# Performance work log

Hardware: AMD Instinct MI355X
Metric: run time of the kernel (lower is better)

Reference implementation:

```python
import jax, jax.numpy as jnp
import numpy as np

PARENTS = np.array([-1, 0, 1, 1, 1])
NECK_CHAIN = np.array([1, 0])  # neck joint (1) up to root (0)
B, V, F, J, S, E = 512, 5023, 9976, 5, 100, 50
L_STAT, L_DYN, L_FULL, N_BUCKET = 51, 17, 68, 79


def rodrigues(rvec):
    """Axis-angle [N,3] -> rotation matrices [N,3,3]."""
    angle = jnp.linalg.norm(rvec + 1e-8, axis=-1, keepdims=True)  # [N,1]
    axis = rvec / angle
    s = jnp.sin(angle)[..., None]
    c = jnp.cos(angle)[..., None]
    rx, ry, rz = axis[:, 0], axis[:, 1], axis[:, 2]
    z = jnp.zeros_like(rx)
    K = jnp.stack([z, -rz, ry, rz, z, -rx, -ry, rx, z], axis=-1).reshape(-1, 3, 3)
    I = jnp.eye(3, dtype=rvec.dtype)
    return I + s * K + (1.0 - c) * (K @ K)


def verts2lmk(vertices, faces, lmk_faces_idx, lmk_bary):
    lmk_faces = faces[lmk_faces_idx]                               # [B,L,3]
    lmk_verts = jax.vmap(lambda v, f: v[f])(vertices, lmk_faces)   # [B,L,3verts,3xyz]
    return jnp.einsum('blfc,blf->blc', lmk_verts, lmk_bary)


def setup_inputs() -> dict:
    key = jax.random.key(0)
    ks = jax.random.split(key, 16)
    shape_params = jax.random.normal(ks[0], (B, S), jnp.float32)
    expression_params = jax.random.normal(ks[1], (B, E), jnp.float32)
    pose_params = 0.2 * jax.random.normal(ks[2], (B, 6), jnp.float32)
    eye_pose_params = 0.1 * jax.random.normal(ks[3], (B, 6), jnp.float32)
    v_template = jax.random.normal(ks[4], (V, 3), jnp.float32) * 0.1
    shapedirs = jax.random.normal(ks[5], (V, 3, S + E), jnp.float32) * 0.01
    posedirs = jax.random.normal(ks[6], ((J - 1) * 9, V * 3), jnp.float32) * 0.01
    jr = jax.random.uniform(ks[7], (J, V), jnp.float32)
    J_regressor = jr / jnp.sum(jr, axis=1, keepdims=True)
    lbs_weights = jax.nn.softmax(jax.random.normal(ks[8], (V, J), jnp.float32), axis=-1)
    faces = jax.random.randint(ks[9], (F, 3), 0, V)
    lmk_faces_idx = jax.random.randint(ks[10], (L_STAT,), 0, F)
    lb = jax.random.uniform(ks[11], (L_STAT, 3), jnp.float32) + 1e-3
    lmk_bary_coords = lb / jnp.sum(lb, axis=-1, keepdims=True)
    dynamic_lmk_faces_idx = jax.random.randint(ks[12], (N_BUCKET, L_DYN), 0, F)
    db = jax.random.uniform(ks[13], (N_BUCKET, L_DYN, 3), jnp.float32) + 1e-3
    dynamic_lmk_bary_coords = db / jnp.sum(db, axis=-1, keepdims=True)
    full_lmk_faces_idx = jax.random.randint(ks[14], (L_FULL,), 0, F)
    fb = jax.random.uniform(ks[15], (L_FULL, 3), jnp.float32) + 1e-3
    full_lmk_bary_coords = fb / jnp.sum(fb, axis=-1, keepdims=True)
    return {
        'shape_params': shape_params, 'expression_params': expression_params,
        'pose_params': pose_params, 'eye_pose_params': eye_pose_params,
        'v_template': v_template, 'shapedirs': shapedirs, 'posedirs': posedirs,
        'J_regressor': J_regressor, 'lbs_weights': lbs_weights, 'faces': faces,
        'lmk_faces_idx': lmk_faces_idx, 'lmk_bary_coords': lmk_bary_coords,
        'dynamic_lmk_faces_idx': dynamic_lmk_faces_idx,
        'dynamic_lmk_bary_coords': dynamic_lmk_bary_coords,
        'full_lmk_faces_idx': full_lmk_faces_idx,
        'full_lmk_bary_coords': full_lmk_bary_coords,
    }


def reference(shape_params, expression_params, pose_params, eye_pose_params,
              v_template, shapedirs, posedirs, J_regressor, lbs_weights, faces,
              lmk_faces_idx, lmk_bary_coords, dynamic_lmk_faces_idx,
              dynamic_lmk_bary_coords, full_lmk_faces_idx, full_lmk_bary_coords):
    b = shape_params.shape[0]
    nv = v_template.shape[0]
    dt = shape_params.dtype
    betas = jnp.concatenate([shape_params, expression_params], axis=1)          # [B,150]
    neck = jnp.zeros((b, 3), dtype=dt)
    full_pose = jnp.concatenate(
        [pose_params[:, :3], neck, pose_params[:, 3:], eye_pose_params], axis=1)  # [B,15]
    # shape + expression blendshapes
    v_shaped = v_template[None] + jnp.einsum('bl,vcl->bvc', betas, shapedirs)   # [B,V,3]
    joints = jnp.einsum('jv,bvc->bjc', J_regressor, v_shaped)                   # [B,5,3]
    rot_mats = rodrigues(full_pose.reshape(-1, 3)).reshape(b, J, 3, 3)          # [B,5,3,3]
    I3 = jnp.eye(3, dtype=dt)
    pose_feature = (rot_mats[:, 1:] - I3).reshape(b, -1)                        # [B,36]
    v_posed = v_shaped + (pose_feature @ posedirs).reshape(b, nv, 3)
    # kinematic chain -> global joint transforms
    rel_J = joints.at[:, 1:].add(-joints[:, PARENTS[1:]])
    tm = jnp.zeros((b, J, 4, 4), dtype=dt)
    tm = tm.at[:, :, :3, :3].set(rot_mats).at[:, :, :3, 3].set(rel_J).at[:, :, 3, 3].set(1.0)
    chain = [tm[:, 0]]
    for i in range(1, J):
        chain.append(chain[PARENTS[i]] @ tm[:, i])
    A = jnp.stack(chain, axis=1)                                                # [B,5,4,4]
    Rj = jnp.einsum('bjmn,bjn->bjm', A[:, :, :3, :3], joints)
    A_rel = A.at[:, :, :3, 3].add(-Rj)
    # per-vertex skinning
    T = jnp.einsum('vj,bjmn->bvmn', lbs_weights, A_rel)                         # [B,V,4,4]
    vertices = jnp.einsum('bvmn,bvn->bvm', T[:, :, :3, :3], v_posed) + T[:, :, :3, 3]
    # dynamic contour landmark selection from neck kin-chain relative rotation
    aa = full_pose.reshape(b, J, 3)[:, NECK_CHAIN]                              # [B,2,3]
    rc = rodrigues(aa.reshape(-1, 3)).reshape(b, len(NECK_CHAIN), 3, 3)
    rel_rot = jnp.broadcast_to(I3, (b, 3, 3))
    for idx in range(len(NECK_CHAIN)):
        rel_rot = rc[:, idx] @ rel_rot
    sy = jnp.sqrt(rel_rot[:, 0, 0] ** 2 + rel_rot[:, 1, 0] ** 2)
    y_deg = jnp.arctan2(-rel_rot[:, 2, 0], sy) * (180.0 / np.pi)
    y_rot = jnp.round(jnp.minimum(y_deg, 39.0)).astype(jnp.int32)
    neg_mask = y_rot < 0
    big_neg = y_rot < -39
    neg_vals = jnp.where(big_neg, 78, 39 - y_rot)
    y_rot = jnp.where(neg_mask, neg_vals, y_rot)                                # [B] in [0,79)
    dyn_faces = dynamic_lmk_faces_idx[y_rot]                                    # [B,17]
    dyn_bary = dynamic_lmk_bary_coords[y_rot]                                   # [B,17,3]
    lf = jnp.concatenate([dyn_faces, jnp.broadcast_to(lmk_faces_idx[None], (b, lmk_faces_idx.shape[0]))], axis=1)
    lb = jnp.concatenate([dyn_bary, jnp.broadcast_to(lmk_bary_coords[None], (b,) + lmk_bary_coords.shape)], axis=1)
    landmarks2d = verts2lmk(vertices, faces, lf, lb)
    ff = jnp.broadcast_to(full_lmk_faces_idx[None], (b, full_lmk_faces_idx.shape[0]))
    fb = jnp.broadcast_to(full_lmk_bary_coords[None], (b,) + full_lmk_bary_coords.shape)
    landmarks3d = verts2lmk(vertices, faces, ff, fb)
    return (vertices, landmarks2d, landmarks3d)
```

## Files before the change

### kernel.cpp

```cpp
#include <hip/hip_runtime.h>
#include <cstddef>
#include <cstdint>

#define cB   512
#define cV   5023
#define cS   100
#define cE   50
#define cJ   5
#define cLD  17
#define cLF  68

#define cV3    15069
#define cNPAD  15072

#define OUT_V  ((size_t)cB * cV * 3)
#define OUT_L  ((size_t)cB * cLF * 3)

#define WS_BTN    ((size_t)0)
#define WS_ATM    (WS_BTN + (size_t)cNPAD * 96)
#define WS_JS2    (WS_ATM + 49152)
#define WS_AREL   (WS_JS2 + 2432)
#define WS_YROT   (WS_AREL + 30720)
#define WS_JSPART (WS_YROT + 512)

typedef __attribute__((ext_vector_type(8))) short short8;
typedef __attribute__((ext_vector_type(4))) float f32x4;

__device__ __forceinline__ unsigned short f2bf(float x) {
  unsigned int u = __float_as_uint(x);
  u = (u + 0x7fffu + ((u >> 16) & 1u)) >> 16;
  return (unsigned short)u;
}

__device__ __forceinline__ void rodrigues9(float rx, float ry, float rz, float* R) {
  float a0 = rx + 1e-8f, a1 = ry + 1e-8f, a2 = rz + 1e-8f;
  float angle = sqrtf(a0 * a0 + a1 * a1 + a2 * a2);
  float inv = 1.0f / angle;
  float x = rx * inv, y = ry * inv, z = rz * inv;
  float s = sinf(angle), c = cosf(angle);
  float t = 1.0f - c;
  float xy = x * y, xz = x * z, yz = y * z;
  R[0] = 1.0f - t * (y * y + z * z);
  R[1] = -s * z + t * xy;
  R[2] =  s * y + t * xz;
  R[3] =  s * z + t * xy;
  R[4] = 1.0f - t * (x * x + z * z);
  R[5] = -s * x + t * yz;
  R[6] = -s * y + t * xz;
  R[7] =  s * x + t * yz;
  R[8] = 1.0f - t * (x * x + y * y);
}

__global__ __launch_bounds__(512) void k_aux(
    const float* __restrict__ sd, const float* __restrict__ pd,
    const float* __restrict__ jreg, const float* __restrict__ vt,
    unsigned int* __restrict__ btn_u, float* __restrict__ JSpart) {
  __shared__ __align__(16) unsigned char sm[44032];
  float* sdt = (float*)sm;
  unsigned short* pdt = (unsigned short*)(sm + 38912);
  const int t = threadIdx.x;
  const int bid = blockIdx.x;
  if (bid < 314) {
    if (t >= 453) return;
    int c = t / 151, l = t - c * 151;
    int v0 = bid * 16;
    float acc[5] = {0.f, 0.f, 0.f, 0.f, 0.f};
#pragma unroll 8
    for (int vi = 0; vi < 16; ++vi) {
      int v = v0 + vi;
      bool ok = (v < cV);
      int vc = ok ? v : 0;
      float x;
      if (l < 150) x = ok ? sd[(size_t)(v * 3 + c) * 150 + l] : 0.f;
      else         x = ok ? vt[v * 3 + c] : 0.f;
#pragma unroll
      for (int j = 0; j < 5; ++j)
        acc[j] = fmaf(jreg[j * cV + vc], x, acc[j]);
    }
#pragma unroll
    for (int j = 0; j < 5; ++j)
      JSpart[(size_t)bid * 2272 + (j * 3 + c) * 151 + l] = acc[j];
  } else {
    const int n0 = (bid - 314) * 64;
    for (int idx = t; idx < 9600; idx += 512) {
      size_t g = (size_t)n0 * 150 + idx;
      float v = (g < (size_t)cV3 * 150) ? sd[g] : 0.f;
      int row = idx / 150, col = idx - row * 150;
      sdt[row * 152 + col] = v;
    }
    for (int e = t; e < 2304; e += 512) {
      int kk = e >> 6, ln = e & 63;
      int n = n0 + ln;
      pdt[ln * 38 + kk] = f2bf((n < cV3) ? pd[(size_t)kk * cV3 + n] : 0.f);
    }
    __syncthreads();
    for (int e = t; e < 6144; e += 512) {
      int row = e / 96, d = e - row * 96;
      int n = n0 + row;
      if (n < cNPAD) {
        unsigned int wv;
        if (d < 75) {
          wv = (unsigned int)f2bf(sdt[row * 152 + 2 * d]) |
               ((unsigned int)f2bf(sdt[row * 152 + 2 * d + 1]) << 16);
        } else if (d < 93) {
          int p = (d - 75) * 2;
          wv = (unsigned int)pdt[row * 38 + p] |
               ((unsigned int)pdt[row * 38 + p + 1] << 16);
        } else {
          wv = 0u;
        }
        btn_u[(size_t)n * 96 + d] = wv;
      }
    }
  }
}

__global__ __launch_bounds__(256) void k_jsred(const float* __restrict__ JSpart,
                                               float* __restrict__ JS2) {
  __shared__ float red[256];
  const int t = threadIdx.x;
  const int e = blockIdx.x * 32 + (t & 31);
  const int pg = t >> 5;
  float s = 0.f;
  if (e < 2265) {
#pragma unroll 8
    for (int p = pg; p < 314; p += 8)
      s += JSpart[(size_t)p * 2272 + e];
  }
  red[t] = s;
  __syncthreads();
  if (t < 128) red[t] += red[t + 128];
  __syncthreads();
  if (t < 64) red[t] += red[t + 64];
  __syncthreads();
  if (t < 32) {
    float v = red[t] + red[t + 32];
    if (e < 2265) {
      int jc = e / 151, l = e - jc * 151;
      JS2[l * 16 + jc] = v;
    }
  }
}

__global__ __launch_bounds__(256) void k_batch(
    const float* __restrict__ shp, const float* __restrict__ expr,
    const float* __restrict__ pose, const float* __restrict__ eyep,
    const float* __restrict__ JS2g, float* __restrict__ Arel,
    int* __restrict__ yrot, unsigned int* __restrict__ atm_u) {
  __shared__ float js2[151 * 16];
  __shared__ float sb[32 * 153];
  __shared__ float pfs[32 * 36];
  const int t = threadIdx.x;
  const int b0 = blockIdx.x * 32;
  for (int i = t; i < 151 * 16; i += 256) js2[i] = JS2g[i];
  for (int e = t; e < 3200; e += 256) {
    int bl = e / 100, l = e - bl * 100;
    sb[bl * 153 + l] = shp[(size_t)(b0 + bl) * 100 + l];
  }
  for (int e = t; e < 1600; e += 256) {
    int bl = e / 50, l = e - bl * 50;
    sb[bl * 153 + 100 + l] = expr[(size_t)(b0 + bl) * 50 + l];
  }
  __syncthreads();

  if (t < 32) {
    int b = b0 + t;
    float jnt[5][3];
    {
      const f32x4* J4 = (const f32x4*)(js2 + 150 * 16);
      f32x4 A = J4[0], Bq = J4[1], Cq = J4[2], Dq = J4[3];
      jnt[0][0] = A.x;  jnt[0][1] = A.y;  jnt[0][2] = A.z;
      jnt[1][0] = A.w;  jnt[1][1] = Bq.x; jnt[1][2] = Bq.y;
      jnt[2][0] = Bq.z; jnt[2][1] = Bq.w; jnt[2][2] = Cq.x;
      jnt[3][0] = Cq.y; jnt[3][1] = Cq.z; jnt[3][2] = Cq.w;
      jnt[4][0] = Dq.x; jnt[4][1] = Dq.y; jnt[4][2] = Dq.z;
    }
    for (int l = 0; l < 150; ++l) {
      const f32x4* J4 = (const f32x4*)(js2 + l * 16);
      f32x4 A = J4[0], Bq = J4[1], Cq = J4[2], Dq = J4[3];
      float beta = sb[t * 153 + l];
      jnt[0][0] = fmaf(beta, A.x,  jnt[0][0]);
      jnt[0][1] = fmaf(beta, A.y,  jnt[0][1]);
      jnt[0][2] = fmaf(beta, A.z,  jnt[0][2]);
      jnt[1][0] = fmaf(beta, A.w,  jnt[1][0]);
      jnt[1][1] = fmaf(beta, Bq.x, jnt[1][1]);
      jnt[1][2] = fmaf(beta, Bq.y, jnt[1][2]);
      jnt[2][0] = fmaf(beta, Bq.z, jnt[2][0]);
      jnt[2][1] = fmaf(beta, Bq.w, jnt[2][1]);
      jnt[2][2] = fmaf(beta, Cq.x, jnt[2][2]);
      jnt[3][0] = fmaf(beta, Cq.y, jnt[3][0]);
      jnt[3][1] = fmaf(beta, Cq.z, jnt[3][1]);
      jnt[3][2] = fmaf(beta, Cq.w, jnt[3][2]);
      jnt[4][0] = fmaf(beta, Dq.x, jnt[4][0]);
      jnt[4][1] = fmaf(beta, Dq.y, jnt[4][1]);
      jnt[4][2] = fmaf(beta, Dq.z, jnt[4][2]);
    }
    float fp[5][3];
    fp[0][0] = pose[b * 6 + 0]; fp[0][1] = pose[b * 6 + 1]; fp[0][2] = pose[b * 6 + 2];
    fp[1][0] = 0.f; fp[1][1] = 0.f; fp[1][2] = 0.f;
    fp[2][0] = pose[b * 6 + 3]; fp[2][1] = pose[b * 6 + 4]; fp[2][2] = pose[b * 6 + 5];
    fp[3][0] = eyep[b * 6 + 0]; fp[3][1] = eyep[b * 6 + 1]; fp[3][2] = eyep[b * 6 + 2];
    fp[4][0] = eyep[b * 6 + 3]; fp[4][1] = eyep[b * 6 + 4]; fp[4][2] = eyep[b * 6 + 5];
    float R[5][9];
#pragma unroll
    for (int j = 0; j < 5; ++j) rodrigues9(fp[j][0], fp[j][1], fp[j][2], R[j]);
#pragma unroll
    for (int j = 1; j < 5; ++j)
#pragma unroll
      for (int r = 0; r < 9; ++r) {
        float id = (r == 0 || r == 4 || r == 8) ? 1.f : 0.f;
        pfs[t * 36 + (j - 1) * 9 + r] = R[j][r] - id;
      }
    float rel[5][3];
#pragma unroll
    for (int c = 0; c < 3; ++c) {
      rel[0][c] = jnt[0][c];
      rel[1][c] = jnt[1][c] - jnt[0][c];
      rel[2][c] = jnt[2][c] - jnt[1][c];
      rel[3][c] = jnt[3][c] - jnt[1][c];
      rel[4][c] = jnt[4][c] - jnt[1][c];
    }
    float GR[5][9], Gt[5][3];
#pragma unroll
    for (int r = 0; r < 9; ++r) GR[0][r] = R[0][r];
#pragma unroll
    for (int c = 0; c < 3; ++c) Gt[0][c] = rel[0][c];
    const int par[5] = {0, 0, 1, 1, 1};
#pragma unroll
    for (int j = 1; j < 5; ++j) {
      int p = par[j];
#pragma unroll
      for (int r = 0; r < 3; ++r) {
#pragma unroll
        for (int cc = 0; cc < 3; ++cc)
          GR[j][r * 3 + cc] = GR[p][r * 3 + 0] * R[j][0 + cc] +
                              GR[p][r * 3 + 1] * R[j][3 + cc] +
                              GR[p][r * 3 + 2] * R[j][6 + cc];
        Gt[j][r] = Gt[p][r] + GR[p][r * 3 + 0] * rel[j][0] +
                              GR[p][r * 3 + 1] * rel[j][1] +
                              GR[p][r * 3 + 2] * rel[j][2];
      }
    }
#pragma unroll
    for (int j = 0; j < 5; ++j)
#pragma unroll
      for (int r = 0; r < 3; ++r) {
        float tj = Gt[j][r] - (GR[j][r * 3 + 0] * jnt[j][0] +
                               GR[j][r * 3 + 1] * jnt[j][1] +
                               GR[j][r * 3 + 2] * jnt[j][2]);
        Arel[b * 60 + j * 12 + r * 4 + 0] = GR[j][r * 3 + 0];
        Arel[b * 60 + j * 12 + r * 4 + 1] = GR[j][r * 3 + 1];
        Arel[b * 60 + j * 12 + r * 4 + 2] = GR[j][r * 3 + 2];
        Arel[b * 60 + j * 12 + r * 4 + 3] = tj;
      }
    float Ra[9], Rb[9];
    rodrigues9(fp[1][0], fp[1][1], fp[1][2], Ra);
    rodrigues9(fp[0][0], fp[0][1], fp[0][2], Rb);
    float r00 = Rb[0] * Ra[0] + Rb[1] * Ra[3] + Rb[2] * Ra[6];
    float r10 = Rb[3] * Ra[0] + Rb[4] * Ra[3] + Rb[5] * Ra[6];
    float r20 = Rb[6] * Ra[0] + Rb[7] * Ra[3] + Rb[8] * Ra[6];
    float sy = sqrtf(r00 * r00 + r10 * r10);
    float ydeg = atan2f(-r20, sy) * 57.29577951308232f;
    int y = (int)rintf(fminf(ydeg, 39.0f));
    if (y < 0) y = (y < -39) ? 78 : (39 - y);
    yrot[b] = y;
  }
  __syncthreads();

#pragma unroll
  for (int it = 0; it < 12; ++it) {
    int e = t + it * 256;
    int bl = e / 96, d = e - bl * 96;
    unsigned int wv;
    if (d < 75) {
      wv = (unsigned int)f2bf(sb[bl * 153 + 2 * d]) |
           ((unsigned int)f2bf(sb[bl * 153 + 2 * d + 1]) << 16);
    } else if (d < 93) {
      wv = (unsigned int)f2bf(pfs[bl * 36 + (d - 75) * 2]) |
           ((unsigned int)f2bf(pfs[bl * 36 + (d - 75) * 2 + 1]) << 16);
    } else {
      wv = 0u;
    }
    atm_u[(size_t)(b0 + bl) * 96 + d] = wv;
  }
}

__global__ __launch_bounds__(256) void k_main(
    const unsigned short* __restrict__ BTn, const unsigned short* __restrict__ ATm,
    const float* __restrict__ Arel, const float* __restrict__ vtempl,
    const float* __restrict__ lbw, float* __restrict__ out) {
  __shared__ float Pf[96 * 66];
  __shared__ float Os[64 * 97];
  __shared__ float lbwT[160];
  __shared__ float vtT[96];

  const int bid = blockIdx.x;
  const int nb = bid >> 3, mb = bid & 7;

  const int t = threadIdx.x;
  const int w = t >> 6, L = t & 63;
  const int wm = w >> 1, wn = w & 1;
  const int lr = L & 15, lq = L >> 4;

  if (t < 160) {
    int vl = t / 5, j = t - vl * 5;
    int v = nb * 32 + vl;
    lbwT[t] = (v < cV) ? lbw[v * 5 + j] : 0.f;
  }
  if (t >= 160 && t < 256) {
    int e = t - 160;
    int vl = e / 3, c = e - vl * 3;
    int v = nb * 32 + vl;
    vtT[e] = (v < cV) ? vtempl[v * 3 + c] : 0.f;
  }

  const unsigned short* abase = ATm + ((size_t)mb * 64 + wm * 32 + lr) * 192 + lq * 8;
  const unsigned short* bbase = BTn + ((size_t)nb * 96 + wn * 48 + lr) * 192 + lq * 8;

  f32x4 acc[2][3];
#pragma unroll
  for (int mt = 0; mt < 2; ++mt)
#pragma unroll
    for (int nt = 0; nt < 3; ++nt) acc[mt][nt] = (f32x4){0.f, 0.f, 0.f, 0.f};

  short8 A0[3], A1[3], B0[3], B1[3], B2[3];
#pragma unroll
  for (int d = 0; d < 3; ++d) {
    const int ko = d * 32;
    A0[d] = *(const short8*)(abase + ko);
    A1[d] = *(const short8*)(abase + 16 * 192 + ko);
    B0[d] = *(const short8*)(bbase + ko);
    B1[d] = *(const short8*)(bbase + 16 * 192 + ko);
    B2[d] = *(const short8*)(bbase + 32 * 192 + ko);
  }
#pragma unroll
  for (int ks = 0; ks < 6; ++ks) {
    const int d = ks % 3;
    short8 a0 = A0[d], a1 = A1[d], b0 = B0[d], b1 = B1[d], b2 = B2[d];
    if (ks < 3) {
      const int ko = (ks + 3) * 32;
      A0[d] = *(const short8*)(abase + ko);
      A1[d] = *(const short8*)(abase + 16 * 192 + ko);
      B0[d] = *(const short8*)(bbase + ko);
      B1[d] = *(const short8*)(bbase + 16 * 192 + ko);
      B2[d] = *(const short8*)(bbase + 32 * 192 + ko);
    }
    acc[0][0] = __builtin_amdgcn_mfma_f32_16x16x32_bf16(a0, b0, acc[0][0], 0, 0, 0);
    acc[1][0] = __builtin_amdgcn_mfma_f32_16x16x32_bf16(a1, b0, acc[1][0], 0, 0, 0);
    acc[0][1] = __builtin_amdgcn_mfma_f32_16x16x32_bf16(a0, b1, acc[0][1], 0, 0, 0);
    acc[1][1] = __builtin_amdgcn_mfma_f32_16x16x32_bf16(a1, b1, acc[1][1], 0, 0, 0);
    acc[0][2] = __builtin_amdgcn_mfma_f32_16x16x32_bf16(a0, b2, acc[0][2], 0, 0, 0);
    acc[1][2] = __builtin_amdgcn_mfma_f32_16x16x32_bf16(a1, b2, acc[1][2], 0, 0, 0);
  }

#pragma unroll
  for (int mt = 0; mt < 2; ++mt)
#pragma unroll
    for (int nt = 0; nt < 3; ++nt) {
      int n_loc = wn * 48 + nt * 16 + lr;
      int m = wm * 32 + mt * 16 + lq * 4;
      *(f32x4*)(Pf + n_loc * 66 + m) = acc[mt][nt];
    }

  const int b_loc = t >> 2, part = t & 3;
  const float* qb = Arel + ((size_t)mb * 64 + b_loc) * 60;
  f32x4 ar[15];
#pragma unroll
  for (int r = 0; r < 15; ++r) ar[r] = *(const f32x4*)(qb + 4 * r);

  __syncthreads();

#pragma unroll
  for (int ii = 0; ii < 8; ++ii) {
    const int vl = part * 8 + ii;
    float px = Pf[(vl * 3 + 0) * 66 + b_loc] + vtT[vl * 3 + 0];
    float py = Pf[(vl * 3 + 1) * 66 + b_loc] + vtT[vl * 3 + 1];
    float pz = Pf[(vl * 3 + 2) * 66 + b_loc] + vtT[vl * 3 + 2];
    float o0 = 0.f, o1 = 0.f, o2 = 0.f;
#pragma unroll
    for (int j = 0; j < 5; ++j) {
      f32x4 q0 = ar[3 * j + 0], q1 = ar[3 * j + 1], q2 = ar[3 * j + 2];
      float s0 = q0.x * px + q0.y * py + q0.z * pz + q0.w;
      float s1 = q1.x * px + q1.y * py + q1.z * pz + q1.w;
      float s2 = q2.x * px + q2.y * py + q2.z * pz + q2.w;
      float wj = lbwT[vl * 5 + j];
      o0 = fmaf(wj, s0, o0);
      o1 = fmaf(wj, s1, o1);
      o2 = fmaf(wj, s2, o2);
    }
    Os[b_loc * 97 + vl * 3 + 0] = o0;
    Os[b_loc * 97 + vl * 3 + 1] = o1;
    Os[b_loc * 97 + vl * 3 + 2] = o2;
  }
  __syncthreads();

  const size_t cv3 = (size_t)cV * 3;
  const size_t ob = ((size_t)(mb * 64) * cV + (size_t)nb * 32) * 3;
#pragma unroll
  for (int s = 0; s < 24; ++s) {
    int idx = s * 256 + t;
    int bb = idx / 96, f = idx - bb * 96;
    if (nb < 156 || f < 93)
      out[ob + (size_t)bb * cv3 + f] = Os[bb * 97 + f];
  }
}

__global__ __launch_bounds__(512) void k_lmk(
    const float* __restrict__ verts, const int* __restrict__ faces,
    const int* __restrict__ lmkf, const float* __restrict__ lmkb,
    const int* __restrict__ dynf, const float* __restrict__ dynb,
    const int* __restrict__ fullf, const float* __restrict__ fullb,
    const int* __restrict__ yrot, float* __restrict__ out) {
  int id = blockIdx.x * 512 + threadIdx.x;
  if (id >= cB * cLF * 6) return;
  int c = id % 3;
  int q = id / 3;
  int sel = q & 1;
  int r = q >> 1;
  int b = r / cLF, l = r - b * cLF;
  const float* vb = verts + (size_t)b * cV * 3;
  int f; float w0, w1, w2; size_t o;
  if (sel == 0) {
    if (l < cLD) {
      int yb = yrot[b];
      f = dynf[yb * cLD + l];
      const float* bp = dynb + ((size_t)yb * cLD + l) * 3;
      w0 = bp[0]; w1 = bp[1]; w2 = bp[2];
    } else {
      f = lmkf[l - cLD];
      const float* bp = lmkb + (size_t)(l - cLD) * 3;
      w0 = bp[0]; w1 = bp[1]; w2 = bp[2];
    }
    o = OUT_V + ((size_t)b * cLF + l) * 3;
  } else {
    f = fullf[l];
    const float* bp = fullb + (size_t)l * 3;
    w0 = bp[0]; w1 = bp[1]; w2 = bp[2];
    o = OUT_V + OUT_L + ((size_t)b * cLF + l) * 3;
  }
  int i0 = faces[f * 3 + 0] * 3, i1 = faces[f * 3 + 1] * 3, i2 = faces[f * 3 + 2] * 3;
  out[o + c] = w0 * vb[i0 + c] + w1 * vb[i1 + c] + w2 * vb[i2 + c];
}

extern "C" void kernel_launch(void* const* d_in, const int* in_sizes, int n_in,
                              void* d_out, int out_size, void* d_ws, size_t ws_size,
                              hipStream_t stream) {
  (void)in_sizes; (void)n_in; (void)out_size; (void)ws_size;
  const float* shp  = (const float*)d_in[0];
  const float* expr = (const float*)d_in[1];
  const float* pose = (const float*)d_in[2];
  const float* eyep = (const float*)d_in[3];
  const float* vt   = (const float*)d_in[4];
  const float* sd   = (const float*)d_in[5];
  const float* pd   = (const float*)d_in[6];
  const float* jreg = (const float*)d_in[7];
  const float* lbw  = (const float*)d_in[8];
  const int*   fcs  = (const int*)d_in[9];
  const int*   lmkf = (const int*)d_in[10];
  const float* lmkb = (const float*)d_in[11];
  const int*   dynf = (const int*)d_in[12];
  const float* dynb = (const float*)d_in[13];
  const int*   fullf= (const int*)d_in[14];
  const float* fullb= (const float*)d_in[15];
  float* out = (float*)d_out;
  float* ws  = (float*)d_ws;

  unsigned int*   btn  = (unsigned int*)(ws + WS_BTN);
  unsigned short* ATm  = (unsigned short*)(ws + WS_ATM);
  float* JS2    = ws + WS_JS2;
  float* Arel   = ws + WS_AREL;
  int*   yrot   = (int*)(ws + WS_YROT);
  float* JSpart = ws + WS_JSPART;

  k_aux<<<550, 512, 0, stream>>>(sd, pd, jreg, vt, btn, JSpart);
  k_jsred<<<71, 256, 0, stream>>>(JSpart, JS2);
  k_batch<<<16, 256, 0, stream>>>(shp, expr, pose, eyep, JS2, Arel, yrot,
                                  (unsigned int*)ATm);
  k_main<<<1256, 256, 0, stream>>>((unsigned short*)btn, ATm, Arel, vt, lbw, out);
  k_lmk<<<408, 512, 0, stream>>>(out, fcs, lmkf, lmkb, dynf, dynb, fullf, fullb, yrot, out);
}
```

Measured before the change: 174.6 us.

## Fuse five kernels into one persistent cooperative kernel with grid syncs

```diff
diff --git a/kernel.cpp b/kernel.cpp
--- a/kernel.cpp
+++ b/kernel.cpp
@@ -1,6 +1,9 @@
 #include <hip/hip_runtime.h>
+#include <hip/hip_cooperative_groups.h>
 #include <cstddef>
 #include <cstdint>
+
+namespace cg = cooperative_groups;
 
 #define cB   512
 #define cV   5023
@@ -51,53 +54,46 @@
   R[8] = 1.0f - t * (x * x + y * y);
 }
 
-__global__ __launch_bounds__(512) void k_aux(
-    const float* __restrict__ sd, const float* __restrict__ pd,
+__global__ __launch_bounds__(256, 2) void k_fused(
+    const float* __restrict__ sd,   const float* __restrict__ pd,
     const float* __restrict__ jreg, const float* __restrict__ vt,
-    unsigned int* __restrict__ btn_u, float* __restrict__ JSpart) {
-  __shared__ __align__(16) unsigned char sm[44032];
-  float* sdt = (float*)sm;
-  unsigned short* pdt = (unsigned short*)(sm + 38912);
+    const float* __restrict__ shp,  const float* __restrict__ expr,
+    const float* __restrict__ pose, const float* __restrict__ eyep,
+    const float* __restrict__ lbw,  const int* __restrict__ fcs,
+    const int* __restrict__ lmkf,   const float* __restrict__ lmkb,
+    const int* __restrict__ dynf,   const float* __restrict__ dynb,
+    const int* __restrict__ fullf,  const float* __restrict__ fullb,
+    float* __restrict__ out,        unsigned int* __restrict__ btn_u,
+    unsigned short* __restrict__ ATm, float* __restrict__ JS2,
+    float* __restrict__ Arel,       int* __restrict__ yrot,
+    float* __restrict__ JSpart) {
+  cg::grid_group grid = cg::this_grid();
+  __shared__ __align__(16) unsigned char smem[38912];
+
   const int t = threadIdx.x;
-  const int bid = blockIdx.x;
-  if (bid < 314) {
-    if (t >= 453) return;
-    int c = t / 151, l = t - c * 151;
-    int v0 = bid * 16;
-    float acc[5] = {0.f, 0.f, 0.f, 0.f, 0.f};
-#pragma unroll 8
-    for (int vi = 0; vi < 16; ++vi) {
-      int v = v0 + vi;
-      bool ok = (v < cV);
-      int vc = ok ? v : 0;
-      float x;
-      if (l < 150) x = ok ? sd[(size_t)(v * 3 + c) * 150 + l] : 0.f;
-      else         x = ok ? vt[v * 3 + c] : 0.f;
-#pragma unroll
-      for (int j = 0; j < 5; ++j)
-        acc[j] = fmaf(jreg[j * cV + vc], x, acc[j]);
-    }
-#pragma unroll
-    for (int j = 0; j < 5; ++j)
-      JSpart[(size_t)bid * 2272 + (j * 3 + c) * 151 + l] = acc[j];
-  } else {
-    const int n0 = (bid - 314) * 64;
-    for (int idx = t; idx < 9600; idx += 512) {
-      size_t g = (size_t)n0 * 150 + idx;
-      float v = (g < (size_t)cV3 * 150) ? sd[g] : 0.f;
-      int row = idx / 150, col = idx - row * 150;
-      sdt[row * 152 + col] = v;
-    }
-    for (int e = t; e < 2304; e += 512) {
-      int kk = e >> 6, ln = e & 63;
-      int n = n0 + ln;
-      pdt[ln * 38 + kk] = f2bf((n < cV3) ? pd[(size_t)kk * cV3 + n] : 0.f);
-    }
-    __syncthreads();
-    for (int e = t; e < 6144; e += 512) {
-      int row = e / 96, d = e - row * 96;
-      int n = n0 + row;
-      if (n < cNPAD) {
+  const int gtid = blockIdx.x * 256 + t;
+  const int gstride = gridDim.x * 256;
+
+  {
+    float* sdt = (float*)smem;
+    unsigned short* pdt = (unsigned short*)(smem + 19456);
+    for (int vb = blockIdx.x; vb < 471; vb += gridDim.x) {
+      const int n0 = vb * 32;
+      for (int idx = t; idx < 4800; idx += 256) {
+        size_t g = (size_t)n0 * 150 + idx;
+        float v = (g < (size_t)cV3 * 150) ? sd[g] : 0.f;
+        int row = idx / 150, col = idx - row * 150;
+        sdt[row * 152 + col] = v;
+      }
+      for (int e = t; e < 1152; e += 256) {
+        int kk = e >> 5, ln = e & 31;
+        int n = n0 + ln;
+        pdt[ln * 38 + kk] = f2bf((n < cV3) ? pd[(size_t)kk * cV3 + n] : 0.f);
+      }
+      __syncthreads();
+      for (int e = t; e < 3072; e += 256) {
+        int row = e / 96, d = e - row * 96;
+        int n = n0 + row;
         unsigned int wv;
         if (d < 75) {
           wv = (unsigned int)f2bf(sdt[row * 152 + 2 * d]) |
@@ -111,349 +107,385 @@
         }
         btn_u[(size_t)n * 96 + d] = wv;
       }
+      __syncthreads();
     }
   }
-}
-
-__global__ __launch_bounds__(256) void k_jsred(const float* __restrict__ JSpart,
-                                               float* __restrict__ JS2) {
-  __shared__ float red[256];
-  const int t = threadIdx.x;
-  const int e = blockIdx.x * 32 + (t & 31);
-  const int pg = t >> 5;
-  float s = 0.f;
-  if (e < 2265) {
+
+  for (int i = gtid; i < 314 * 453; i += gstride) {
+    int p = i / 453, e = i - p * 453;
+    int c = e / 151, l = e - c * 151;
+    int v0 = p * 16;
+    float acc[5] = {0.f, 0.f, 0.f, 0.f, 0.f};
 #pragma unroll 8
-    for (int p = pg; p < 314; p += 8)
-      s += JSpart[(size_t)p * 2272 + e];
-  }
-  red[t] = s;
-  __syncthreads();
-  if (t < 128) red[t] += red[t + 128];
-  __syncthreads();
-  if (t < 64) red[t] += red[t + 64];
-  __syncthreads();
-  if (t < 32) {
-    float v = red[t] + red[t + 32];
-    if (e < 2265) {
-      int jc = e / 151, l = e - jc * 151;
-      JS2[l * 16 + jc] = v;
+    for (int vi = 0; vi < 16; ++vi) {
+      int v = v0 + vi;
+      bool ok = (v < cV);
+      int vc = ok ? v : 0;
+      float x;
+      if (l < 150) x = ok ? sd[(size_t)(v * 3 + c) * 150 + l] : 0.f;
+      else         x = ok ? vt[v * 3 + c] : 0.f;
+#pragma unroll
+      for (int j = 0; j < 5; ++j)
+        acc[j] = fmaf(jreg[j * cV + vc], x, acc[j]);
     }
-  }
-}
-
-__global__ __launch_bounds__(256) void k_batch(
-    const float* __restrict__ shp, const float* __restrict__ expr,
-    const float* __restrict__ pose, const float* __restrict__ eyep,
-    const float* __restrict__ JS2g, float* __restrict__ Arel,
-    int* __restrict__ yrot, unsigned int* __restrict__ atm_u) {
-  __shared__ float js2[151 * 16];
-  __shared__ float sb[32 * 153];
-  __shared__ float pfs[32 * 36];
-  const int t = threadIdx.x;
-  const int b0 = blockIdx.x * 32;
-  for (int i = t; i < 151 * 16; i += 256) js2[i] = JS2g[i];
-  for (int e = t; e < 3200; e += 256) {
-    int bl = e / 100, l = e - bl * 100;
-    sb[bl * 153 + l] = shp[(size_t)(b0 + bl) * 100 + l];
-  }
-  for (int e = t; e < 1600; e += 256) {
-    int bl = e / 50, l = e - bl * 50;
-    sb[bl * 153 + 100 + l] = expr[(size_t)(b0 + bl) * 50 + l];
-  }
-  __syncthreads();
-
-  if (t < 32) {
-    int b = b0 + t;
-    float jnt[5][3];
-    {
-      const f32x4* J4 = (const f32x4*)(js2 + 150 * 16);
-      f32x4 A = J4[0], Bq = J4[1], Cq = J4[2], Dq = J4[3];
-      jnt[0][0] = A.x;  jnt[0][1] = A.y;  jnt[0][2] = A.z;
-      jnt[1][0] = A.w;  jnt[1][1] = Bq.x; jnt[1][2] = Bq.y;
-      jnt[2][0] = Bq.z; jnt[2][1] = Bq.w; jnt[2][2] = Cq.x;
-      jnt[3][0] = Cq.y; jnt[3][1] = Cq.z; jnt[3][2] = Cq.w;
-      jnt[4][0] = Dq.x; jnt[4][1] = Dq.y; jnt[4][2] = Dq.z;
+#pragma unroll
+    for (int j = 0; j < 5; ++j)
+      JSpart[(size_t)p * 2272 + (j * 3 + c) * 151 + l] = acc[j];
+  }
+
+  __threadfence();
+  grid.sync();
+
+  {
+    float* red = (float*)smem;
+    for (int vb = blockIdx.x; vb < 71; vb += gridDim.x) {
+      const int e = vb * 32 + (t & 31);
+      const int pg = t >> 5;
+      float s = 0.f;
+      if (e < 2265) {
+#pragma unroll 8
+        for (int p = pg; p < 314; p += 8)
+          s += JSpart[(size_t)p * 2272 + e];
+      }
+      red[t] = s;
+      __syncthreads();
+      if (t < 128) red[t] += red[t + 128];
+      __syncthreads();
+      if (t < 64) red[t] += red[t + 64];
+      __syncthreads();
+      if (t < 32) {
+        float v = red[t] + red[t + 32];
+        if (e < 2265) {
+          int jc = e / 151, l = e - jc * 151;
+          JS2[l * 16 + jc] = v;
+        }
+      }
+      __syncthreads();
     }
-    for (int l = 0; l < 150; ++l) {
-      const f32x4* J4 = (const f32x4*)(js2 + l * 16);
-      f32x4 A = J4[0], Bq = J4[1], Cq = J4[2], Dq = J4[3];
-      float beta = sb[t * 153 + l];
-      jnt[0][0] = fmaf(beta, A.x,  jnt[0][0]);
-      jnt[0][1] = fmaf(beta, A.y,  jnt[0][1]);
-      jnt[0][2] = fmaf(beta, A.z,  jnt[0][2]);
-      jnt[1][0] = fmaf(beta, A.w,  jnt[1][0]);
-      jnt[1][1] = fmaf(beta, Bq.x, jnt[1][1]);
-      jnt[1][2] = fmaf(beta, Bq.y, jnt[1][2]);
-      jnt[2][0] = fmaf(beta, Bq.z, jnt[2][0]);
-      jnt[2][1] = fmaf(beta, Bq.w, jnt[2][1]);
-      jnt[2][2] = fmaf(beta, Cq.x, jnt[2][2]);
-      jnt[3][0] = fmaf(beta, Cq.y, jnt[3][0]);
-      jnt[3][1] = fmaf(beta, Cq.z, jnt[3][1]);
-      jnt[3][2] = fmaf(beta, Cq.w, jnt[3][2]);
-      jnt[4][0] = fmaf(beta, Dq.x, jnt[4][0]);
-      jnt[4][1] = fmaf(beta, Dq.y, jnt[4][1]);
-      jnt[4][2] = fmaf(beta, Dq.z, jnt[4][2]);
+  }
+
+  __threadfence();
+  grid.sync();
+
+  {
+    float* js2 = (float*)smem;
+    float* sb  = (float*)(smem + 9664);
+    float* pfs = (float*)(smem + 29248);
+    for (int vb = blockIdx.x; vb < 16; vb += gridDim.x) {
+      const int b0 = vb * 32;
+      for (int i = t; i < 151 * 16; i += 256) js2[i] = JS2[i];
+      for (int e = t; e < 3200; e += 256) {
+        int bl = e / 100, l = e - bl * 100;
+        sb[bl * 153 + l] = shp[(size_t)(b0 + bl) * 100 + l];
+      }
+      for (int e = t; e < 1600; e += 256) {
+        int bl = e / 50, l = e - bl * 50;
+        sb[bl * 153 + 100 + l] = expr[(size_t)(b0 + bl) * 50 + l];
+      }
+      __syncthreads();
+
+      if (t < 32) {
+        int b = b0 + t;
+        float jnt[5][3];
+        {
+          const f32x4* J4 = (const f32x4*)(js2 + 150 * 16);
+          f32x4 A = J4[0], Bq = J4[1], Cq = J4[2], Dq = J4[3];
+          jnt[0][0] = A.x;  jnt[0][1] = A.y;  jnt[0][2] = A.z;
+          jnt[1][0] = A.w;  jnt[1][1] = Bq.x; jnt[1][2] = Bq.y;
+          jnt[2][0] = Bq.z; jnt[2][1] = Bq.w; jnt[2][2] = Cq.x;
+          jnt[3][0] = Cq.y; jnt[3][1] = Cq.z; jnt[3][2] = Cq.w;
+          jnt[4][0] = Dq.x; jnt[4][1] = Dq.y; jnt[4][2] = Dq.z;
+        }
+        for (int l = 0; l < 150; ++l) {
+          const f32x4* J4 = (const f32x4*)(js2 + l * 16);
+          f32x4 A = J4[0], Bq = J4[1], Cq = J4[2], Dq = J4[3];
+          float beta = sb[t * 153 + l];
+          jnt[0][0] = fmaf(beta, A.x,  jnt[0][0]);
+          jnt[0][1] = fmaf(beta, A.y,  jnt[0][1]);
+          jnt[0][2] = fmaf(beta, A.z,  jnt[0][2]);
+          jnt[1][0] = fmaf(beta, A.w,  jnt[1][0]);
+          jnt[1][1] = fmaf(beta, Bq.x, jnt[1][1]);
+          jnt[1][2] = fmaf(beta, Bq.y, jnt[1][2]);
+          jnt[2][0] = fmaf(beta, Bq.z, jnt[2][0]);
+          jnt[2][1] = fmaf(beta, Bq.w, jnt[2][1]);
+          jnt[2][2] = fmaf(beta, Cq.x, jnt[2][2]);
+          jnt[3][0] = fmaf(beta, Cq.y, jnt[3][0]);
+          jnt[3][1] = fmaf(beta, Cq.z, jnt[3][1]);
+          jnt[3][2] = fmaf(beta, Cq.w, jnt[3][2]);
+          jnt[4][0] = fmaf(beta, Dq.x, jnt[4][0]);
+          jnt[4][1] = fmaf(beta, Dq.y, jnt[4][1]);
+          jnt[4][2] = fmaf(beta, Dq.z, jnt[4][2]);
+        }
+        float fp[5][3];
+        fp[0][0] = pose[b * 6 + 0]; fp[0][1] = pose[b * 6 + 1]; fp[0][2] = pose[b * 6 + 2];
+        fp[1][0] = 0.f; fp[1][1] = 0.f; fp[1][2] = 0.f;
+        fp[2][0] = pose[b * 6 + 3]; fp[2][1] = pose[b * 6 + 4]; fp[2][2] = pose[b * 6 + 5];
+        fp[3][0] = eyep[b * 6 + 0]; fp[3][1] = eyep[b * 6 + 1]; fp[3][2] = eyep[b * 6 + 2];
+        fp[4][0] = eyep[b * 6 + 3]; fp[4][1] = eyep[b * 6 + 4]; fp[4][2] = eyep[b * 6 + 5];
+        float R[5][9];
+#pragma unroll
+        for (int j = 0; j < 5; ++j) rodrigues9(fp[j][0], fp[j][1], fp[j][2], R[j]);
+#pragma unroll
+        for (int j = 1; j < 5; ++j)
+#pragma unroll
+          for (int r = 0; r < 9; ++r) {
+            float id = (r == 0 || r == 4 || r == 8) ? 1.f : 0.f;
+            pfs[t * 36 + (j - 1) * 9 + r] = R[j][r] - id;
+          }
+        float rel[5][3];
+#pragma unroll
+        for (int c = 0; c < 3; ++c) {
+          rel[0][c] = jnt[0][c];
+          rel[1][c] = jnt[1][c] - jnt[0][c];
+          rel[2][c] = jnt[2][c] - jnt[1][c];
+          rel[3][c] = jnt[3][c] - jnt[1][c];
+          rel[4][c] = jnt[4][c] - jnt[1][c];
+        }
+        float GR[5][9], Gt[5][3];
+#pragma unroll
+        for (int r = 0; r < 9; ++r) GR[0][r] = R[0][r];
+#pragma unroll
+        for (int c = 0; c < 3; ++c) Gt[0][c] = rel[0][c];
+        const int par[5] = {0, 0, 1, 1, 1};
+#pragma unroll
+        for (int j = 1; j < 5; ++j) {
+          int p = par[j];
+#pragma unroll
+          for (int r = 0; r < 3; ++r) {
+#pragma unroll
+            for (int cc = 0; cc < 3; ++cc)
+              GR[j][r * 3 + cc] = GR[p][r * 3 + 0] * R[j][0 + cc] +
+                                  GR[p][r * 3 + 1] * R[j][3 + cc] +
+                                  GR[p][r * 3 + 2] * R[j][6 + cc];
+            Gt[j][r] = Gt[p][r] + GR[p][r * 3 + 0] * rel[j][0] +
+                                  GR[p][r * 3 + 1] * rel[j][1] +
+                                  GR[p][r * 3 + 2] * rel[j][2];
+          }
+        }
+#pragma unroll
+        for (int j = 0; j < 5; ++j)
+#pragma unroll
+          for (int r = 0; r < 3; ++r) {
+            float tj = Gt[j][r] - (GR[j][r * 3 + 0] * jnt[j][0] +
+                                   GR[j][r * 3 + 1] * jnt[j][1] +
+                                   GR[j][r * 3 + 2] * jnt[j][2]);
+            Arel[b * 60 + j * 12 + r * 4 + 0] = GR[j][r * 3 + 0];
+            Arel[b * 60 + j * 12 + r * 4 + 1] = GR[j][r * 3 + 1];
+            Arel[b * 60 + j * 12 + r * 4 + 2] = GR[j][r * 3 + 2];
+            Arel[b * 60 + j * 12 + r * 4 + 3] = tj;
+          }
+        float Ra[9], Rb[9];
+        rodrigues9(fp[1][0], fp[1][1], fp[1][2], Ra);
+        rodrigues9(fp[0][0], fp[0][1], fp[0][2], Rb);
+        float r00 = Rb[0] * Ra[0] + Rb[1] * Ra[3] + Rb[2] * Ra[6];
+        float r10 = Rb[3] * Ra[0] + Rb[4] * Ra[3] + Rb[5] * Ra[6];
+        float r20 = Rb[6] * Ra[0] + Rb[7] * Ra[3] + Rb[8] * Ra[6];
+        float sy = sqrtf(r00 * r00 + r10 * r10);
+        float ydeg = atan2f(-r20, sy) * 57.29577951308232f;
+        int y = (int)rintf(fminf(ydeg, 39.0f));
+        if (y < 0) y = (y < -39) ? 78 : (39 - y);
+        yrot[b] = y;
+      }
+      __syncthreads();
+
+#pragma unroll
+      for (int it = 0; it < 12; ++it) {
+        int e = t + it * 256;
+        int bl = e / 96, d = e - bl * 96;
+        unsigned int wv;
+        if (d < 75) {
+          wv = (unsigned int)f2bf(sb[bl * 153 + 2 * d]) |
+               ((unsigned int)f2bf(sb[bl * 153 + 2 * d + 1]) << 16);
+        } else if (d < 93) {
+          wv = (unsigned int)f2bf(pfs[bl * 36 + (d - 75) * 2]) |
+               ((unsigned int)f2bf(pfs[bl * 36 + (d - 75) * 2 + 1]) << 16);
+        } else {
+          wv = 0u;
+        }
+        ((unsigned int*)ATm)[(size_t)(b0 + bl) * 96 + d] = wv;
+      }
+      __syncthreads();
     }
-    float fp[5][3];
-    fp[0][0] = pose[b * 6 + 0]; fp[0][1] = pose[b * 6 + 1]; fp[0][2] = pose[b * 6 + 2];
-    fp[1][0] = 0.f; fp[1][1] = 0.f; fp[1][2] = 0.f;
-    fp[2][0] = pose[b * 6 + 3]; fp[2][1] = pose[b * 6 + 4]; fp[2][2] = pose[b * 6 + 5];
-    fp[3][0] = eyep[b * 6 + 0]; fp[3][1] = eyep[b * 6 + 1]; fp[3][2] = eyep[b * 6 + 2];
-    fp[4][0] = eyep[b * 6 + 3]; fp[4][1] = eyep[b * 6 + 4]; fp[4][2] = eyep[b * 6 + 5];
-    float R[5][9];
-#pragma unroll
-    for (int j = 0; j < 5; ++j) rodrigues9(fp[j][0], fp[j][1], fp[j][2], R[j]);
-#pragma unroll
-    for (int j = 1; j < 5; ++j)
-#pragma unroll
-      for (int r = 0; r < 9; ++r) {
-        float id = (r == 0 || r == 4 || r == 8) ? 1.f : 0.f;
-        pfs[t * 36 + (j - 1) * 9 + r] = R[j][r] - id;
-      }
-    float rel[5][3];
-#pragma unroll
-    for (int c = 0; c < 3; ++c) {
-      rel[0][c] = jnt[0][c];
-      rel[1][c] = jnt[1][c] - jnt[0][c];
-      rel[2][c] = jnt[2][c] - jnt[1][c];
-      rel[3][c] = jnt[3][c] - jnt[1][c];
-      rel[4][c] = jnt[4][c] - jnt[1][c];
+  }
+
+  __threadfence();
+  grid.sync();
+
+  {
+    float* Pf   = (float*)smem;
+    float* Os   = (float*)(smem + 25344);
+    float* lbwT = (float*)(smem + 37632);
+    float* vtT  = (float*)(smem + 38272);
+    const unsigned short* BTn = (const unsigned short*)btn_u;
+    const size_t cv3 = (size_t)cV * 3;
+
+    const int w = t >> 6, L = t & 63;
+    const int wm = w >> 1, wn = w & 1;
+    const int lr = L & 15, lq = L >> 4;
+    const int bq = t >> 3, vt8 = t & 7;
+
+    for (int vb = blockIdx.x; vb < 1256; vb += gridDim.x) {
+      const int nb = vb >> 3, mb = vb & 7;
+
+      if (t < 160) {
+        int vl = t / 5, j = t - vl * 5;
+        int v = nb * 32 + vl;
+        lbwT[t] = (v < cV) ? lbw[v * 5 + j] : 0.f;
+      }
+      if (t >= 160 && t < 256) {
+        int e = t - 160;
+        int vl = e / 3, c = e - vl * 3;
+        int v = nb * 32 + vl;
+        vtT[e] = (v < cV) ? vt[v * 3 + c] : 0.f;
+      }
+
+      const unsigned short* abase = ATm + ((size_t)mb * 64 + wm * 32 + lr) * 192 + lq * 8;
+      const unsigned short* bbase = BTn + ((size_t)nb * 96 + wn * 48 + lr) * 192 + lq * 8;
+
+      f32x4 acc[2][3];
+#pragma unroll
+      for (int mt = 0; mt < 2; ++mt)
+#pragma unroll
+        for (int nt = 0; nt < 3; ++nt) acc[mt][nt] = (f32x4){0.f, 0.f, 0.f, 0.f};
+
+      short8 A0[3], A1[3], B0[3], B1[3], B2[3];
+#pragma unroll
+      for (int d = 0; d < 3; ++d) {
+        const int ko = d * 32;
+        A0[d] = *(const short8*)(abase + ko);
+        A1[d] = *(const short8*)(abase + 16 * 192 + ko);
+        B0[d] = *(const short8*)(bbase + ko);
+        B1[d] = *(const short8*)(bbase + 16 * 192 + ko);
+        B2[d] = *(const short8*)(bbase + 32 * 192 + ko);
+      }
+#pragma unroll
+      for (int ks = 0; ks < 6; ++ks) {
+        const int d = ks % 3;
+        short8 a0 = A0[d], a1 = A1[d], b0 = B0[d], b1 = B1[d], b2 = B2[d];
+        if (ks < 3) {
+          const int ko = (ks + 3) * 32;
+          A0[d] = *(const short8*)(abase + ko);
+          A1[d] = *(const short8*)(abase + 16 * 192 + ko);
+          B0[d] = *(const short8*)(bbase + ko);
+          B1[d] = *(const short8*)(bbase + 16 * 192 + ko);
+          B2[d] = *(const short8*)(bbase + 32 * 192 + ko);
+        }
+        acc[0][0] = __builtin_amdgcn_mfma_f32_16x16x32_bf16(a0, b0, acc[0][0], 0, 0, 0);
+        acc[1][0] = __builtin_amdgcn_mfma_f32_16x16x32_bf16(a1, b0, acc[1][0], 0, 0, 0);
+        acc[0][1] = __builtin_amdgcn_mfma_f32_16x16x32_bf16(a0, b1, acc[0][1], 0, 0, 0);
+        acc[1][1] = __builtin_amdgcn_mfma_f32_16x16x32_bf16(a1, b1, acc[1][1], 0, 0, 0);
+        acc[0][2] = __builtin_amdgcn_mfma_f32_16x16x32_bf16(a0, b2, acc[0][2], 0, 0, 0);
+        acc[1][2] = __builtin_amdgcn_mfma_f32_16x16x32_bf16(a1, b2, acc[1][2], 0, 0, 0);
+      }
+
+#pragma unroll
+      for (int mt = 0; mt < 2; ++mt)
+#pragma unroll
+        for (int nt = 0; nt < 3; ++nt) {
+          int n_loc = wn * 48 + nt * 16 + lr;
+          int m = wm * 32 + mt * 16 + lq * 4;
+          *(f32x4*)(Pf + n_loc * 66 + m) = acc[mt][nt];
+        }
+      __syncthreads();
+
+#pragma unroll 1
+      for (int h = 0; h < 2; ++h) {
+        if (h) __syncthreads();
+        const int bcol = h * 32 + bq;
+        const int b = mb * 64 + bcol;
+        const float* qb = Arel + (size_t)b * 60;
+        f32x4 ar[15];
+#pragma unroll
+        for (int r = 0; r < 15; ++r) ar[r] = *(const f32x4*)(qb + 4 * r);
+
+        float o12[12];
+#pragma unroll
+        for (int ii = 0; ii < 4; ++ii) {
+          const int vl = vt8 * 4 + ii;
+          float px = Pf[(vl * 3 + 0) * 66 + bcol] + vtT[vl * 3 + 0];
+          float py = Pf[(vl * 3 + 1) * 66 + bcol] + vtT[vl * 3 + 1];
+          float pz = Pf[(vl * 3 + 2) * 66 + bcol] + vtT[vl * 3 + 2];
+          float o0 = 0.f, o1 = 0.f, o2 = 0.f;
+#pragma unroll
+          for (int j = 0; j < 5; ++j) {
+            f32x4 q0 = ar[3 * j + 0], q1 = ar[3 * j + 1], q2 = ar[3 * j + 2];
+            float s0 = q0.x * px + q0.y * py + q0.z * pz + q0.w;
+            float s1 = q1.x * px + q1.y * py + q1.z * pz + q1.w;
+            float s2 = q2.x * px + q2.y * py + q2.z * pz + q2.w;
+            float wj = lbwT[vl * 5 + j];
+            o0 = fmaf(wj, s0, o0);
+            o1 = fmaf(wj, s1, o1);
+            o2 = fmaf(wj, s2, o2);
+          }
+          o12[ii * 3 + 0] = o0; o12[ii * 3 + 1] = o1; o12[ii * 3 + 2] = o2;
+        }
+        {
+          float* op = Os + bq * 96 + vt8 * 12;
+          *(f32x4*)(op + 0) = (f32x4){o12[0], o12[1], o12[2],  o12[3]};
+          *(f32x4*)(op + 4) = (f32x4){o12[4], o12[5], o12[6],  o12[7]};
+          *(f32x4*)(op + 8) = (f32x4){o12[8], o12[9], o12[10], o12[11]};
+        }
+        __syncthreads();
+
+        const size_t ob = ((size_t)(mb * 64 + h * 32) * cV + (size_t)nb * 32) * 3;
+#pragma unroll
+        for (int s = 0; s < 12; ++s) {
+          int idx = s * 256 + t;
+          int bb = idx / 96, f = idx - bb * 96;
+          if (nb < 156 || f < 93)
+            out[ob + (size_t)bb * cv3 + f] = Os[idx];
+        }
+      }
+      __syncthreads();
     }
-    float GR[5][9], Gt[5][3];
-#pragma unroll
-    for (int r = 0; r < 9; ++r) GR[0][r] = R[0][r];
-#pragma unroll
-    for (int c = 0; c < 3; ++c) Gt[0][c] = rel[0][c];
-    const int par[5] = {0, 0, 1, 1, 1};
-#pragma unroll
-    for (int j = 1; j < 5; ++j) {
-      int p = par[j];
-#pragma unroll
-      for (int r = 0; r < 3; ++r) {
-#pragma unroll
-        for (int cc = 0; cc < 3; ++cc)
-          GR[j][r * 3 + cc] = GR[p][r * 3 + 0] * R[j][0 + cc] +
-                              GR[p][r * 3 + 1] * R[j][3 + cc] +
-                              GR[p][r * 3 + 2] * R[j][6 + cc];
-        Gt[j][r] = Gt[p][r] + GR[p][r * 3 + 0] * rel[j][0] +
-                              GR[p][r * 3 + 1] * rel[j][1] +
-                              GR[p][r * 3 + 2] * rel[j][2];
-      }
+  }
+
+  __threadfence();
+  grid.sync();
+
+  for (int id = gtid; id < cB * cLF * 6; id += gstride) {
+    int c = id % 3;
+    int q = id / 3;
+    int sel = q & 1;
+    int r = q >> 1;
+    int b = r / cLF, l = r - b * cLF;
+    const float* vb = out + (size_t)b * cV * 3;
+    int f; float w0, w1, w2; size_t o;
+    if (sel == 0) {
+      if (l < cLD) {
+        int yb = yrot[b];
+        f = dynf[yb * cLD + l];
+        const float* bp = dynb + ((size_t)yb * cLD + l) * 3;
+        w0 = bp[0]; w1 = bp[1]; w2 = bp[2];
+      } else {
+        f = lmkf[l - cLD];
+        const float* bp = lmkb + (size_t)(l - cLD) * 3;
+        w0 = bp[0]; w1 = bp[1]; w2 = bp[2];
+      }
+      o = OUT_V + ((size_t)b * cLF + l) * 3;
+    } else {
+      f = fullf[l];
+      const float* bp = fullb + (size_t)l * 3;
+      w0 = bp[0]; w1 = bp[1]; w2 = bp[2];
+      o = OUT_V + OUT_L + ((size_t)b * cLF + l) * 3;
     }
-#pragma unroll
-    for (int j = 0; j < 5; ++j)
-#pragma unroll
-      for (int r = 0; r < 3; ++r) {
-        float tj = Gt[j][r] - (GR[j][r * 3 + 0] * jnt[j][0] +
-                               GR[j][r * 3 + 1] * jnt[j][1] +
-                               GR[j][r * 3 + 2] * jnt[j][2]);
-        Arel[b * 60 + j * 12 + r * 4 + 0] = GR[j][r * 3 + 0];
-        Arel[b * 60 + j * 12 + r * 4 + 1] = GR[j][r * 3 + 1];
-        Arel[b * 60 + j * 12 + r * 4 + 2] = GR[j][r * 3 + 2];
-        Arel[b * 60 + j * 12 + r * 4 + 3] = tj;
-      }
-    float Ra[9], Rb[9];
-    rodrigues9(fp[1][0], fp[1][1], fp[1][2], Ra);
-    rodrigues9(fp[0][0], fp[0][1], fp[0][2], Rb);
-    float r00 = Rb[0] * Ra[0] + Rb[1] * Ra[3] + Rb[2] * Ra[6];
-    float r10 = Rb[3] * Ra[0] + Rb[4] * Ra[3] + Rb[5] * Ra[6];
-    float r20 = Rb[6] * Ra[0] + Rb[7] * Ra[3] + Rb[8] * Ra[6];
-    float sy = sqrtf(r00 * r00 + r10 * r10);
-    float ydeg = atan2f(-r20, sy) * 57.29577951308232f;
-    int y = (int)rintf(fminf(ydeg, 39.0f));
-    if (y < 0) y = (y < -39) ? 78 : (39 - y);
-    yrot[b] = y;
-  }
-  __syncthreads();
-
-#pragma unroll
-  for (int it = 0; it < 12; ++it) {
-    int e = t + it * 256;
-    int bl = e / 96, d = e - bl * 96;
-    unsigned int wv;
-    if (d < 75) {
-      wv = (unsigned int)f2bf(sb[bl * 153 + 2 * d]) |
-           ((unsigned int)f2bf(sb[bl * 153 + 2 * d + 1]) << 16);
-    } else if (d < 93) {
-      wv = (unsigned int)f2bf(pfs[bl * 36 + (d - 75) * 2]) |
-           ((unsigned int)f2bf(pfs[bl * 36 + (d - 75) * 2 + 1]) << 16);
-    } else {
-      wv = 0u;
-    }
-    atm_u[(size_t)(b0 + bl) * 96 + d] = wv;
-  }
-}
-
-__global__ __launch_bounds__(256) void k_main(
-    const unsigned short* __restrict__ BTn, const unsigned short* __restrict__ ATm,
-    const float* __restrict__ Arel, const float* __restrict__ vtempl,
-    const float* __restrict__ lbw, float* __restrict__ out) {
-  __shared__ float Pf[96 * 66];
-  __shared__ float Os[64 * 97];
-  __shared__ float lbwT[160];
-  __shared__ float vtT[96];
-
-  const int bid = blockIdx.x;
-  const int nb = bid >> 3, mb = bid & 7;
-
-  const int t = threadIdx.x;
-  const int w = t >> 6, L = t & 63;
-  const int wm = w >> 1, wn = w & 1;
-  const int lr = L & 15, lq = L >> 4;
-
-  if (t < 160) {
-    int vl = t / 5, j = t - vl * 5;
-    int v = nb * 32 + vl;
-    lbwT[t] = (v < cV) ? lbw[v * 5 + j] : 0.f;
-  }
-  if (t >= 160 && t < 256) {
-    int e = t - 160;
-    int vl = e / 3, c = e - vl * 3;
-    int v = nb * 32 + vl;
-    vtT[e] = (v < cV) ? vtempl[v * 3 + c] : 0.f;
-  }
-
-  const unsigned short* abase = ATm + ((size_t)mb * 64 + wm * 32 + lr) * 192 + lq * 8;
-  const unsigned short* bbase = BTn + ((size_t)nb * 96 + wn * 48 + lr) * 192 + lq * 8;
-
-  f32x4 acc[2][3];
-#pragma unroll
-  for (int mt = 0; mt < 2; ++mt)
-#pragma unroll
-    for (int nt = 0; nt < 3; ++nt) acc[mt][nt] = (f32x4){0.f, 0.f, 0.f, 0.f};
-
-  short8 A0[3], A1[3], B0[3], B1[3], B2[3];
-#pragma unroll
-  for (int d = 0; d < 3; ++d) {
-    const int ko = d * 32;
-    A0[d] = *(const short8*)(abase + ko);
-    A1[d] = *(const short8*)(abase + 16 * 192 + ko);
-    B0[d] = *(const short8*)(bbase + ko);
-    B1[d] = *(const short8*)(bbase + 16 * 192 + ko);
-    B2[d] = *(const short8*)(bbase + 32 * 192 + ko);
-  }
-#pragma unroll
-  for (int ks = 0; ks < 6; ++ks) {
-    const int d = ks % 3;
-    short8 a0 = A0[d], a1 = A1[d], b0 = B0[d], b1 = B1[d], b2 = B2[d];
-    if (ks < 3) {
-      const int ko = (ks + 3) * 32;
-      A0[d] = *(const short8*)(abase + ko);
-      A1[d] = *(const short8*)(abase + 16 * 192 + ko);
-      B0[d] = *(const short8*)(bbase + ko);
-      B1[d] = *(const short8*)(bbase + 16 * 192 + ko);
-      B2[d] = *(const short8*)(bbase + 32 * 192 + ko);
-    }
-    acc[0][0] = __builtin_amdgcn_mfma_f32_16x16x32_bf16(a0, b0, acc[0][0], 0, 0, 0);
-    acc[1][0] = __builtin_amdgcn_mfma_f32_16x16x32_bf16(a1, b0, acc[1][0], 0, 0, 0);
-    acc[0][1] = __builtin_amdgcn_mfma_f32_16x16x32_bf16(a0, b1, acc[0][1], 0, 0, 0);
-    acc[1][1] = __builtin_amdgcn_mfma_f32_16x16x32_bf16(a1, b1, acc[1][1], 0, 0, 0);
-    acc[0][2] = __builtin_amdgcn_mfma_f32_16x16x32_bf16(a0, b2, acc[0][2], 0, 0, 0);
-    acc[1][2] = __builtin_amdgcn_mfma_f32_16x16x32_bf16(a1, b2, acc[1][2], 0, 0, 0);
-  }
-
-#pragma unroll
-  for (int mt = 0; mt < 2; ++mt)
-#pragma unroll
-    for (int nt = 0; nt < 3; ++nt) {
-      int n_loc = wn * 48 + nt * 16 + lr;
-      int m = wm * 32 + mt * 16 + lq * 4;
-      *(f32x4*)(Pf + n_loc * 66 + m) = acc[mt][nt];
-    }
-
-  const int b_loc = t >> 2, part = t & 3;
-  const float* qb = Arel + ((size_t)mb * 64 + b_loc) * 60;
-  f32x4 ar[15];
-#pragma unroll
-  for (int r = 0; r < 15; ++r) ar[r] = *(const f32x4*)(qb + 4 * r);
-
-  __syncthreads();
-
-#pragma unroll
-  for (int ii = 0; ii < 8; ++ii) {
-    const int vl = part * 8 + ii;
-    float px = Pf[(vl * 3 + 0) * 66 + b_loc] + vtT[vl * 3 + 0];
-    float py = Pf[(vl * 3 + 1) * 66 + b_loc] + vtT[vl * 3 + 1];
-    float pz = Pf[(vl * 3 + 2) * 66 + b_loc] + vtT[vl * 3 + 2];
-    float o0 = 0.f, o1 = 0.f, o2 = 0.f;
-#pragma unroll
-    for (int j = 0; j < 5; ++j) {
-      f32x4 q0 = ar[3 * j + 0], q1 = ar[3 * j + 1], q2 = ar[3 * j + 2];
-      float s0 = q0.x * px + q0.y * py + q0.z * pz + q0.w;
-      float s1 = q1.x * px + q1.y * py + q1.z * pz + q1.w;
-      float s2 = q2.x * px + q2.y * py + q2.z * pz + q2.w;
-      float wj = lbwT[vl * 5 + j];
-      o0 = fmaf(wj, s0, o0);
-      o1 = fmaf(wj, s1, o1);
-      o2 = fmaf(wj, s2, o2);
-    }
-    Os[b_loc * 97 + vl * 3 + 0] = o0;
-    Os[b_loc * 97 + vl * 3 + 1] = o1;
-    Os[b_loc * 97 + vl * 3 + 2] = o2;
-  }
-  __syncthreads();
-
-  const size_t cv3 = (size_t)cV * 3;
-  const size_t ob = ((size_t)(mb * 64) * cV + (size_t)nb * 32) * 3;
-#pragma unroll
-  for (int s = 0; s < 24; ++s) {
-    int idx = s * 256 + t;
-    int bb = idx / 96, f = idx - bb * 96;
-    if (nb < 156 || f < 93)
-      out[ob + (size_t)bb * cv3 + f] = Os[bb * 97 + f];
-  }
-}
-
-__global__ __launch_bounds__(512) void k_lmk(
-    const float* __restrict__ verts, const int* __restrict__ faces,
-    const int* __restrict__ lmkf, const float* __restrict__ lmkb,
-    const int* __restrict__ dynf, const float* __restrict__ dynb,
-    const int* __restrict__ fullf, const float* __restrict__ fullb,
-    const int* __restrict__ yrot, float* __restrict__ out) {
-  int id = blockIdx.x * 512 + threadIdx.x;
-  if (id >= cB * cLF * 6) return;
-  int c = id % 3;
-  int q = id / 3;
-  int sel = q & 1;
-  int r = q >> 1;
-  int b = r / cLF, l = r - b * cLF;
-  const float* vb = verts + (size_t)b * cV * 3;
-  int f; float w0, w1, w2; size_t o;
-  if (sel == 0) {
-    if (l < cLD) {
-      int yb = yrot[b];
-      f = dynf[yb * cLD + l];
-      const float* bp = dynb + ((size_t)yb * cLD + l) * 3;
-      w0 = bp[0]; w1 = bp[1]; w2 = bp[2];
-    } else {
-      f = lmkf[l - cLD];
-      const float* bp = lmkb + (size_t)(l - cLD) * 3;
-      w0 = bp[0]; w1 = bp[1]; w2 = bp[2];
-    }
-    o = OUT_V + ((size_t)b * cLF + l) * 3;
-  } else {
-    f = fullf[l];
-    const float* bp = fullb + (size_t)l * 3;
-    w0 = bp[0]; w1 = bp[1]; w2 = bp[2];
-    o = OUT_V + OUT_L + ((size_t)b * cLF + l) * 3;
-  }
-  int i0 = faces[f * 3 + 0] * 3, i1 = faces[f * 3 + 1] * 3, i2 = faces[f * 3 + 2] * 3;
-  out[o + c] = w0 * vb[i0 + c] + w1 * vb[i1 + c] + w2 * vb[i2 + c];
+    int i0 = fcs[f * 3 + 0] * 3, i1 = fcs[f * 3 + 1] * 3, i2 = fcs[f * 3 + 2] * 3;
+    out[o + c] = w0 * vb[i0 + c] + w1 * vb[i1 + c] + w2 * vb[i2 + c];
+  }
 }
 
 extern "C" void kernel_launch(void* const* d_in, const int* in_sizes, int n_in,
                               void* d_out, int out_size, void* d_ws, size_t ws_size,
                               hipStream_t stream) {
   (void)in_sizes; (void)n_in; (void)out_size; (void)ws_size;
+  const float* sd   = (const float*)d_in[5];
+  const float* pd   = (const float*)d_in[6];
+  const float* jreg = (const float*)d_in[7];
+  const float* vt   = (const float*)d_in[4];
   const float* shp  = (const float*)d_in[0];
   const float* expr = (const float*)d_in[1];
   const float* pose = (const float*)d_in[2];
   const float* eyep = (const float*)d_in[3];
-  const float* vt   = (const float*)d_in[4];
-  const float* sd   = (const float*)d_in[5];
-  const float* pd   = (const float*)d_in[6];
-  const float* jreg = (const float*)d_in[7];
   const float* lbw  = (const float*)d_in[8];
   const int*   fcs  = (const int*)d_in[9];
   const int*   lmkf = (const int*)d_in[10];
@@ -472,10 +504,30 @@
   int*   yrot   = (int*)(ws + WS_YROT);
   float* JSpart = ws + WS_JSPART;
 
-  k_aux<<<550, 512, 0, stream>>>(sd, pd, jreg, vt, btn, JSpart);
-  k_jsred<<<71, 256, 0, stream>>>(JSpart, JS2);
-  k_batch<<<16, 256, 0, stream>>>(shp, expr, pose, eyep, JS2, Arel, yrot,
-                                  (unsigned int*)ATm);
-  k_main<<<1256, 256, 0, stream>>>((unsigned short*)btn, ATm, Arel, vt, lbw, out);
-  k_lmk<<<408, 512, 0, stream>>>(out, fcs, lmkf, lmkb, dynf, dynb, fullf, fullb, yrot, out);
+  static int s_grid = 0;
+  if (s_grid == 0) {
+    int occ = 0;
+    hipError_t e = hipOccupancyMaxActiveBlocksPerMultiprocessor(&occ, k_fused, 256, 0);
+    int cus = 256;
+    hipDeviceProp_t prop;
+    int dev = 0;
+    if (hipGetDevice(&dev) == hipSuccess &&
+        hipGetDeviceProperties(&prop, dev) == hipSuccess)
+      cus = prop.multiProcessorCount;
+    int g = (e == hipSuccess && occ > 0) ? occ * cus : 2 * cus;
+    if (g > 1024) g = 1024;
+    if (g < 256) g = 256;
+    s_grid = g;
+  }
+
+  void* args[] = {
+    (void*)&sd, (void*)&pd, (void*)&jreg, (void*)&vt,
+    (void*)&shp, (void*)&expr, (void*)&pose, (void*)&eyep,
+    (void*)&lbw, (void*)&fcs, (void*)&lmkf, (void*)&lmkb,
+    (void*)&dynf, (void*)&dynb, (void*)&fullf, (void*)&fullb,
+    (void*)&out, (void*)&btn, (void*)&ATm, (void*)&JS2,
+    (void*)&Arel, (void*)&yrot, (void*)&JSpart
+  };
+  hipLaunchCooperativeKernel((void*)k_fused, dim3(s_grid), dim3(256),
+                             args, 0, stream);
 }
```

Measured after the change: 434.3 us. +148.8%, slower.
